# Performance work log

Measured on AMD Instinct MI355X. Metric: run time of the kernel, lower is better.

## Reference

```python
import jax, jax.numpy as jnp
import numpy as np

D_MODEL = 256
D_INNER = 512   # expand_factor * d_model
D_STATE = 64
DT_RANK = 4     # ceil(d_model / 64)
D_CONV = 4
B = 8
L = 144


def setup_inputs() -> dict:
    key = jax.random.key(0)
    ks = jax.random.split(key, 8)
    s = lambda k, shp, sc=0.02: jax.random.normal(k, shp, jnp.float32) * sc
    x = jax.random.normal(ks[0], (B, L, D_MODEL), jnp.float32)
    lastin = jnp.zeros((B, D_INNER, D_STATE), jnp.float32)  # accepted but unused by the scan
    W_in = s(ks[1], (2 * D_INNER, D_MODEL))              # in_proj (no bias)
    conv_w = s(ks[2], (D_INNER, 1, D_CONV), 0.1)          # depthwise conv kernel [O, I/groups, K]
    conv_b = jnp.zeros((D_INNER,), jnp.float32)
    W_x = s(ks[3], (DT_RANK + 2 * D_STATE, D_INNER))      # x_proj (no bias)
    W_dt = s(ks[4], (D_INNER, DT_RANK), 0.1)
    b_dt = jnp.full((D_INNER,), -4.0, jnp.float32)        # softplus -> small dt, like mamba init
    A_log = jnp.log(jnp.tile(jnp.arange(1, D_STATE + 1, dtype=jnp.float32), (D_INNER, 1)))
    Dp = jnp.ones((D_INNER,), jnp.float32)
    W_out = s(ks[5], (D_MODEL, D_INNER))                  # out_proj (no bias)
    return dict(x=x, lastin=lastin, W_in=W_in, conv_w=conv_w, conv_b=conv_b,
                W_x=W_x, W_dt=W_dt, b_dt=b_dt, A_log=A_log, Dp=Dp, W_out=W_out)


def _forward(x, lastin, W_in, conv_w, conv_b, W_x, W_dt, b_dt, A_log, Dp, W_out):
    # in_proj and split
    xz = jnp.einsum('bld,ed->ble', x, W_in)               # [B, L, 2*d_inner]
    ix, z = jnp.split(xz, 2, axis=-1)

    # depthwise causal-ish conv1d: torch padding=2 then slice [:L] == padding (2, 1)
    ix = jnp.swapaxes(ix, 1, 2)                            # [B, d_inner, L]
    ix = jax.lax.conv_general_dilated(
        ix, conv_w, window_strides=(1,), padding=[(2, 1)],
        feature_group_count=D_INNER, dimension_numbers=('NCH', 'OIH', 'NCH'))
    ix = ix + conv_b[None, :, None]
    ix = jnp.swapaxes(ix, 1, 2)                            # [B, L, d_inner]
    ix = jax.nn.silu(ix)

    # ssm parameterization
    A = -jnp.exp(A_log)                                    # [d_inner, d_state]
    dBC = jnp.einsum('bld,ed->ble', ix, W_x)               # [B, L, dt_rank + 2*d_state]
    dt_r = dBC[..., :DT_RANK]
    Bm = dBC[..., DT_RANK:DT_RANK + D_STATE]               # [B, L, d_state]
    Cm = dBC[..., DT_RANK + D_STATE:]                      # [B, L, d_state]
    delta = jax.nn.softplus(jnp.einsum('blr,dr->bld', dt_r, W_dt) + b_dt)  # [B, L, d_inner]

    # discretization
    deltaA = jnp.exp(delta[..., None] * A)                 # [B, L, d_inner, d_state]
    BX = (delta * ix)[..., None] * Bm[:, :, None, :]       # [B, L, d_inner, d_state]

    # sequential selective scan: h_t = deltaA_t * h_{t-1} + BX_t
    def step(h, inp):
        dA_t, bx_t = inp
        h = dA_t * h + bx_t
        return h, h

    h0 = jnp.zeros((x.shape[0], D_INNER, D_STATE), x.dtype)
    _, hs = jax.lax.scan(step, h0, (jnp.moveaxis(deltaA, 1, 0), jnp.moveaxis(BX, 1, 0)))
    # hs: [L, B, d_inner, d_state]

    y = jnp.einsum('lbdn,lbn->bld', hs, jnp.moveaxis(Cm, 1, 0))  # [B, L, d_inner]
    y = y + Dp * ix

    out = jnp.einsum('bld,ed->ble', y * jax.nn.silu(z), W_out)   # [B, L, d_model]
    return out


def reference(x, lastin, W_in, conv_w, conv_b, W_x, W_dt, b_dt, A_log, Dp, W_out):
    return _forward(x, lastin, W_in, conv_w, conv_b, W_x, W_dt, b_dt, A_log, Dp, W_out)
```

## Files before the change

### kernel.cpp

```cpp
#include <hip/hip_runtime.h>
#include <hip/hip_bf16.h>

#define B_SZ 8
#define L_SEQ 144
#define NTOK 1152
#define D_MODEL 256
#define D_INNER 512
#define D_STATE 64
#define DT_RANK 4

#define BM 64
#define BN 64
#define BK 16

template<bool A_MK, bool B_NK, bool GN>
__global__ __launch_bounds__(256) void gemm_k(const float* __restrict__ A,
                                              const float* __restrict__ Bm,
                                              float* __restrict__ C,
                                              const int M, const int N, const int K,
                                              const int lda, const int ldb, const int ldc,
                                              const int kslab, const size_t sstride) {
    __shared__ float As[BK][BM + 4];
    __shared__ float Bs[BK][BN + 4];
    const int tid = threadIdx.x;
    const int m0 = blockIdx.y * BM;
    const int n0 = blockIdx.x * BN;
    const int kbeg = blockIdx.z * kslab;
    const int kend = kbeg + kslab;
    const int ty = tid >> 4, tx = tid & 15;
    const int lrow = tid >> 2, kq = (tid & 3) * 4;
    const int kk = tid >> 4, cc = (tid & 15) * 4;
    float acc[4][4] = {};

    for (int k0 = kbeg; k0 < kend; k0 += BK) {
        float4 av, bv;
        if (A_MK) av = *(const float4*)(A + (size_t)(m0 + lrow) * lda + k0 + kq);
        else      av = *(const float4*)(A + (size_t)(k0 + kk) * lda + m0 + cc);
        if (B_NK) {
            bv = *(const float4*)(Bm + (size_t)(k0 + kk) * ldb + n0 + cc);
        } else {
            bv = make_float4(0.f, 0.f, 0.f, 0.f);
            if (!GN || (n0 + lrow) < N)
                bv = *(const float4*)(Bm + (size_t)(n0 + lrow) * ldb + k0 + kq);
        }
        __syncthreads();
        if (A_MK) {
            As[kq + 0][lrow] = av.x; As[kq + 1][lrow] = av.y;
            As[kq + 2][lrow] = av.z; As[kq + 3][lrow] = av.w;
        } else {
            *(float4*)&As[kk][cc] = av;
        }
        if (B_NK) {
            *(float4*)&Bs[kk][cc] = bv;
        } else {
            Bs[kq + 0][lrow] = bv.x; Bs[kq + 1][lrow] = bv.y;
            Bs[kq + 2][lrow] = bv.z; Bs[kq + 3][lrow] = bv.w;
        }
        __syncthreads();
#pragma unroll
        for (int k = 0; k < BK; ++k) {
            const float4 a4 = *(const float4*)&As[k][ty * 4];
            const float4 b4 = *(const float4*)&Bs[k][tx * 4];
            const float a_[4] = {a4.x, a4.y, a4.z, a4.w};
            const float b_[4] = {b4.x, b4.y, b4.z, b4.w};
#pragma unroll
            for (int i = 0; i < 4; ++i)
#pragma unroll
                for (int j = 0; j < 4; ++j)
                    acc[i][j] = fmaf(a_[i], b_[j], acc[i][j]);
        }
    }
    C += (size_t)blockIdx.z * sstride;
#pragma unroll
    for (int i = 0; i < 4; ++i) {
        const int gm = m0 + ty * 4 + i;
        const int gn = n0 + tx * 4;
        if (!GN || gn < N)
            *(float4*)(C + (size_t)gm * ldc + gn) =
                make_float4(acc[i][0], acc[i][1], acc[i][2], acc[i][3]);
    }
}

__global__ __launch_bounds__(256) void reduce4_k(const float4* __restrict__ in,
                                                 float4* __restrict__ out,
                                                 const int n4, const int s4) {
    const int i = blockIdx.x * 256 + threadIdx.x;
    if (i >= n4) return;
    const float4 a = in[i], b = in[i + s4], c = in[i + 2 * s4], d = in[i + 3 * s4];
    out[i] = make_float4(a.x + b.x + c.x + d.x, a.y + b.y + c.y + d.y,
                         a.z + b.z + c.z + d.z, a.w + b.w + c.w + d.w);
}

__global__ __launch_bounds__(128) void conv_k(const float* __restrict__ xzT,
                                              const float* __restrict__ cw,
                                              const float* __restrict__ cb,
                                              float* __restrict__ ixT) {
    const int tok = blockIdx.x * 128 + threadIdx.x;
    const int d = blockIdx.y;
    const int b = tok / L_SEQ;
    const int t = tok - b * L_SEQ;
    const float* row = xzT + (size_t)d * NTOK + tok;
    const float4 w = *(const float4*)(cw + d * 4);
    float s = cb[d];
    if (t >= 2) s = fmaf(w.x, row[-2], s);
    if (t >= 1) s = fmaf(w.y, row[-1], s);
    s = fmaf(w.z, row[0], s);
    if (t < L_SEQ - 1) s = fmaf(w.w, row[1], s);
    ixT[(size_t)d * NTOK + tok] = s * __builtin_amdgcn_rcpf(1.f + __expf(-s));
}

template<int CNT>
__device__ __forceinline__ void scan_chunk(const float* __restrict__ dBC,
                                           const float* __restrict__ xzT,
                                           const float* __restrict__ ixT,
                                           float* __restrict__ gT,
                                           float4* __restrict__ aux_w,
                                           float (*__restrict__ Pw)[65],
                                           const int d, const int base, const int t0,
                                           const float An2, const float4 wdt,
                                           const float bdt, const float dpv,
                                           const int lane, float& h) {
    if (lane < CNT) {
        const int tok = base + t0 + lane;
        const float4 dt4 = *(const float4*)(dBC + (size_t)tok * 132);
        float s = fmaf(dt4.x, wdt.x, bdt);
        s = fmaf(dt4.y, wdt.y, s);
        s = fmaf(dt4.z, wdt.z, s);
        s = fmaf(dt4.w, wdt.w, s);
        const float delta = fmaxf(s, 0.f) + __logf(1.f + __expf(-fabsf(s)));
        const float ixv = ixT[(size_t)d * NTOK + tok];
        const float zv  = xzT[(size_t)(D_INNER + d) * NTOK + tok];
        const float sz  = zv * __builtin_amdgcn_rcpf(1.f + __expf(-zv));
        aux_w[lane] = make_float4(delta, delta * ixv, dpv * ixv, sz);
    }
#pragma unroll 8
    for (int i = 0; i < CNT; ++i) {
        const size_t rb = (size_t)(base + t0 + i) * 132;
        const float Bv = dBC[rb + DT_RANK + lane];
        const float Cv = dBC[rb + DT_RANK + D_STATE + lane];
        const float4 a4 = aux_w[i];
        const float dA = __builtin_amdgcn_exp2f(a4.x * An2);
        h = fmaf(dA, h, a4.y * Bv);
        Pw[i][lane] = h * Cv;
    }
    const int tl = lane & 31, hf = lane >> 5;
    float s2 = 0.f;
    if (tl < CNT) {
#pragma unroll
        for (int j = 0; j < 32; ++j) s2 += Pw[tl][hf * 32 + j];
    }
    s2 += __shfl_xor(s2, 32, 64);
    if (hf == 0 && tl < CNT) {
        const float4 a4 = aux_w[tl];
        gT[(size_t)d * NTOK + base + t0 + tl] = (s2 + a4.z) * a4.w;
    }
}

__global__ __launch_bounds__(256) void scan_k(const float* __restrict__ dBC,
                                              const float* __restrict__ xzT,
                                              const float* __restrict__ ixT,
                                              const float* __restrict__ W_dt,
                                              const float* __restrict__ b_dt,
                                              const float* __restrict__ A_log,
                                              const float* __restrict__ Dp,
                                              float* __restrict__ gT) {
    __shared__ float4 aux_s[4][32];
    __shared__ float P[4][32][65];
    const int w = threadIdx.x >> 6, lane = threadIdx.x & 63;
    const int b = blockIdx.x >> 7, dg = blockIdx.x & 127;
    const int d = (dg << 2) | w;
    const int base = b * L_SEQ;
    const float An2 = -__expf(A_log[(d << 6) + lane]) * 1.44269504088896f;
    const float4 wdt = *(const float4*)(W_dt + (d << 2));
    const float bdt = b_dt[d], dpv = Dp[d];
    float h = 0.f;
    scan_chunk<32>(dBC, xzT, ixT, gT, aux_s[w], P[w], d, base, 0,  An2, wdt, bdt, dpv, lane, h);
    scan_chunk<32>(dBC, xzT, ixT, gT, aux_s[w], P[w], d, base, 32, An2, wdt, bdt, dpv, lane, h);
    scan_chunk<32>(dBC, xzT, ixT, gT, aux_s[w], P[w], d, base, 64, An2, wdt, bdt, dpv, lane, h);
    scan_chunk<32>(dBC, xzT, ixT, gT, aux_s[w], P[w], d, base, 96, An2, wdt, bdt, dpv, lane, h);
    scan_chunk<16>(dBC, xzT, ixT, gT, aux_s[w], P[w], d, base, 128, An2, wdt, bdt, dpv, lane, h);
}

extern "C" void kernel_launch(void* const* d_in, const int* in_sizes, int n_in,
                              void* d_out, int out_size, void* d_ws, size_t ws_size,
                              hipStream_t stream) {
    const float* x      = (const float*)d_in[0];
    const float* W_in   = (const float*)d_in[2];
    const float* conv_w = (const float*)d_in[3];
    const float* conv_b = (const float*)d_in[4];
    const float* W_x    = (const float*)d_in[5];
    const float* W_dt   = (const float*)d_in[6];
    const float* b_dt   = (const float*)d_in[7];
    const float* A_log  = (const float*)d_in[8];
    const float* Dp     = (const float*)d_in[9];
    const float* W_out  = (const float*)d_in[10];
    float* out = (float*)d_out;

    float* ws    = (float*)d_ws;
    float* xzT   = ws;
    float* ixT   = xzT + 1179648;
    float* dBC   = ixT + 589824;
    float* gT    = dBC + 152064;
    float* slab3 = gT + 589824;
    float* slab6 = xzT;

    gemm_k<true, false, false><<<dim3(18, 16, 1), 256, 0, stream>>>(
        W_in, x, xzT, 1024, NTOK, D_MODEL, D_MODEL, D_MODEL, NTOK, D_MODEL, 0);
    conv_k<<<dim3(9, D_INNER), 128, 0, stream>>>(xzT, conv_w, conv_b, ixT);
    gemm_k<false, false, true><<<dim3(3, 18, 4), 256, 0, stream>>>(
        ixT, W_x, slab3, NTOK, 132, D_INNER, NTOK, D_INNER, 132, 128, (size_t)NTOK * 132);
    reduce4_k<<<dim3(149), 256, 0, stream>>>((const float4*)slab3, (float4*)dBC,
                                             NTOK * 132 / 4, NTOK * 132 / 4);
    scan_k<<<dim3(B_SZ * 128), 256, 0, stream>>>(dBC, xzT, ixT, W_dt, b_dt, A_log, Dp, gT);
    gemm_k<false, false, false><<<dim3(4, 18, 4), 256, 0, stream>>>(
        gT, W_out, slab6, NTOK, D_MODEL, D_INNER, NTOK, D_INNER, D_MODEL, 128,
        (size_t)NTOK * D_MODEL);
    reduce4_k<<<dim3(288), 256, 0, stream>>>((const float4*)slab6, (float4*)out,
                                             NTOK * D_MODEL / 4, NTOK * D_MODEL / 4);
}
```

Baseline: 141.0 us.

## Replace FP32 SIMT GEMMs with split-bf16 MFMA GEMMs and transpose-pack kernels

Swaps the scalar FP32 tiled GEMM for an MFMA kernel that splits each FP32 operand into high and low bf16 parts and accumulates three bf16 products, approximating FP32 accuracy on matrix cores. The activations for the x_proj and out_proj GEMMs are first transposed and packed into hi/lo bf16 pairs by a new transpack kernel. The split-K slabs and reduce kernels are removed. This adds two transpose passes and loses some precision compared with true FP32, and the GEMMs now run without split-K, so they launch fewer blocks.

```diff
diff --git a/kernel.cpp b/kernel.cpp
--- a/kernel.cpp
+++ b/kernel.cpp
@@ -9,86 +9,150 @@
 #define D_STATE 64
 #define DT_RANK 4
 
-#define BM 64
-#define BN 64
-#define BK 16
-
-template<bool A_MK, bool B_NK, bool GN>
-__global__ __launch_bounds__(256) void gemm_k(const float* __restrict__ A,
-                                              const float* __restrict__ Bm,
-                                              float* __restrict__ C,
-                                              const int M, const int N, const int K,
-                                              const int lda, const int ldb, const int ldc,
-                                              const int kslab, const size_t sstride) {
-    __shared__ float As[BK][BM + 4];
-    __shared__ float Bs[BK][BN + 4];
+typedef __attribute__((ext_vector_type(8))) short bf16x8;
+typedef __attribute__((ext_vector_type(4))) float f32x4;
+typedef __attribute__((ext_vector_type(4))) short short4v;
+
+__device__ __forceinline__ unsigned short bf16_rn(float f) {
+    unsigned u = __float_as_uint(f);
+    u += 0x7FFF + ((u >> 16) & 1);
+    return (unsigned short)(u >> 16);
+}
+__device__ __forceinline__ float bf16_f(unsigned short h) {
+    return __uint_as_float(((unsigned)h) << 16);
+}
+__device__ __forceinline__ unsigned packsplit(float f) {
+    const unsigned short h = bf16_rn(f);
+    const unsigned short l = bf16_rn(f - bf16_f(h));
+    return (unsigned)h | ((unsigned)l << 16);
+}
+
+#define LP 40
+
+template<bool APACK, bool GN>
+__global__ __launch_bounds__(256) void gemm_mfma(const void* __restrict__ Aptr,
+                                                 const float* __restrict__ Bptr,
+                                                 float* __restrict__ C,
+                                                 const int N, const int K,
+                                                 const int lda, const int ldb,
+                                                 const int ldc) {
+    __shared__ short Ah[64 * LP], Al[64 * LP], Bh[64 * LP], Bl[64 * LP];
+    const float* Af = (const float*)Aptr;
+    const unsigned* Au = (const unsigned*)Aptr;
     const int tid = threadIdx.x;
-    const int m0 = blockIdx.y * BM;
-    const int n0 = blockIdx.x * BN;
-    const int kbeg = blockIdx.z * kslab;
-    const int kend = kbeg + kslab;
-    const int ty = tid >> 4, tx = tid & 15;
-    const int lrow = tid >> 2, kq = (tid & 3) * 4;
-    const int kk = tid >> 4, cc = (tid & 15) * 4;
-    float acc[4][4] = {};
-
-    for (int k0 = kbeg; k0 < kend; k0 += BK) {
-        float4 av, bv;
-        if (A_MK) av = *(const float4*)(A + (size_t)(m0 + lrow) * lda + k0 + kq);
-        else      av = *(const float4*)(A + (size_t)(k0 + kk) * lda + m0 + cc);
-        if (B_NK) {
-            bv = *(const float4*)(Bm + (size_t)(k0 + kk) * ldb + n0 + cc);
-        } else {
-            bv = make_float4(0.f, 0.f, 0.f, 0.f);
-            if (!GN || (n0 + lrow) < N)
-                bv = *(const float4*)(Bm + (size_t)(n0 + lrow) * ldb + k0 + kq);
+    const int m0 = blockIdx.y * 64;
+    const int n0 = blockIdx.x * 64;
+    const int w = tid >> 6, l = tid & 63;
+    const int lm = l & 15, lq = l >> 4;
+    const int m0w = (w >> 1) * 32, n0w = (w & 1) * 32;
+    f32x4 acc[2][2] = {};
+
+    for (int k0 = 0; k0 < K; k0 += 32) {
+        unsigned short ha[2][4], la[2][4], hb[2][4], lb[2][4];
+#pragma unroll
+        for (int p = 0; p < 2; ++p) {
+            const int i = tid + 256 * p;
+            const int r = i >> 3, c = (i & 7) * 4;
+            if (APACK) {
+                const uint4 v = *(const uint4*)(Au + (size_t)(m0 + r) * lda + k0 + c);
+                ha[p][0] = v.x & 0xFFFF; la[p][0] = v.x >> 16;
+                ha[p][1] = v.y & 0xFFFF; la[p][1] = v.y >> 16;
+                ha[p][2] = v.z & 0xFFFF; la[p][2] = v.z >> 16;
+                ha[p][3] = v.w & 0xFFFF; la[p][3] = v.w >> 16;
+            } else {
+                const float4 v = *(const float4*)(Af + (size_t)(m0 + r) * lda + k0 + c);
+                ha[p][0] = bf16_rn(v.x); la[p][0] = bf16_rn(v.x - bf16_f(ha[p][0]));
+                ha[p][1] = bf16_rn(v.y); la[p][1] = bf16_rn(v.y - bf16_f(ha[p][1]));
+                ha[p][2] = bf16_rn(v.z); la[p][2] = bf16_rn(v.z - bf16_f(ha[p][2]));
+                ha[p][3] = bf16_rn(v.w); la[p][3] = bf16_rn(v.w - bf16_f(ha[p][3]));
+            }
+            float4 bv = make_float4(0.f, 0.f, 0.f, 0.f);
+            if (!GN || (n0 + r) < N)
+                bv = *(const float4*)(Bptr + (size_t)(n0 + r) * ldb + k0 + c);
+            hb[p][0] = bf16_rn(bv.x); lb[p][0] = bf16_rn(bv.x - bf16_f(hb[p][0]));
+            hb[p][1] = bf16_rn(bv.y); lb[p][1] = bf16_rn(bv.y - bf16_f(hb[p][1]));
+            hb[p][2] = bf16_rn(bv.z); lb[p][2] = bf16_rn(bv.z - bf16_f(hb[p][2]));
+            hb[p][3] = bf16_rn(bv.w); lb[p][3] = bf16_rn(bv.w - bf16_f(hb[p][3]));
         }
         __syncthreads();
-        if (A_MK) {
-            As[kq + 0][lrow] = av.x; As[kq + 1][lrow] = av.y;
-            As[kq + 2][lrow] = av.z; As[kq + 3][lrow] = av.w;
-        } else {
-            *(float4*)&As[kk][cc] = av;
-        }
-        if (B_NK) {
-            *(float4*)&Bs[kk][cc] = bv;
-        } else {
-            Bs[kq + 0][lrow] = bv.x; Bs[kq + 1][lrow] = bv.y;
-            Bs[kq + 2][lrow] = bv.z; Bs[kq + 3][lrow] = bv.w;
+#pragma unroll
+        for (int p = 0; p < 2; ++p) {
+            const int i = tid + 256 * p;
+            const int r = i >> 3, c = (i & 7) * 4;
+            const int o = r * LP + c;
+            short4v v;
+            v = (short4v){(short)ha[p][0], (short)ha[p][1], (short)ha[p][2], (short)ha[p][3]};
+            *(short4v*)&Ah[o] = v;
+            v = (short4v){(short)la[p][0], (short)la[p][1], (short)la[p][2], (short)la[p][3]};
+            *(short4v*)&Al[o] = v;
+            v = (short4v){(short)hb[p][0], (short)hb[p][1], (short)hb[p][2], (short)hb[p][3]};
+            *(short4v*)&Bh[o] = v;
+            v = (short4v){(short)lb[p][0], (short)lb[p][1], (short)lb[p][2], (short)lb[p][3]};
+            *(short4v*)&Bl[o] = v;
         }
         __syncthreads();
-#pragma unroll
-        for (int k = 0; k < BK; ++k) {
-            const float4 a4 = *(const float4*)&As[k][ty * 4];
-            const float4 b4 = *(const float4*)&Bs[k][tx * 4];
-            const float a_[4] = {a4.x, a4.y, a4.z, a4.w};
-            const float b_[4] = {b4.x, b4.y, b4.z, b4.w};
-#pragma unroll
-            for (int i = 0; i < 4; ++i)
-#pragma unroll
-                for (int j = 0; j < 4; ++j)
-                    acc[i][j] = fmaf(a_[i], b_[j], acc[i][j]);
-        }
-    }
-    C += (size_t)blockIdx.z * sstride;
-#pragma unroll
-    for (int i = 0; i < 4; ++i) {
-        const int gm = m0 + ty * 4 + i;
-        const int gn = n0 + tx * 4;
-        if (!GN || gn < N)
-            *(float4*)(C + (size_t)gm * ldc + gn) =
-                make_float4(acc[i][0], acc[i][1], acc[i][2], acc[i][3]);
-    }
-}
-
-__global__ __launch_bounds__(256) void reduce4_k(const float4* __restrict__ in,
-                                                 float4* __restrict__ out,
-                                                 const int n4, const int s4) {
-    const int i = blockIdx.x * 256 + threadIdx.x;
-    if (i >= n4) return;
-    const float4 a = in[i], b = in[i + s4], c = in[i + 2 * s4], d = in[i + 3 * s4];
-    out[i] = make_float4(a.x + b.x + c.x + d.x, a.y + b.y + c.y + d.y,
-                         a.z + b.z + c.z + d.z, a.w + b.w + c.w + d.w);
+        bf16x8 fah[2], fal[2], fbh[2], fbl[2];
+#pragma unroll
+        for (int t = 0; t < 2; ++t) {
+            const int ao = (m0w + t * 16 + lm) * LP + lq * 8;
+            fah[t] = *(const bf16x8*)&Ah[ao];
+            fal[t] = *(const bf16x8*)&Al[ao];
+            const int bo = (n0w + t * 16 + lm) * LP + lq * 8;
+            fbh[t] = *(const bf16x8*)&Bh[bo];
+            fbl[t] = *(const bf16x8*)&Bl[bo];
+        }
+#pragma unroll
+        for (int mt = 0; mt < 2; ++mt)
+#pragma unroll
+            for (int nt = 0; nt < 2; ++nt) {
+                acc[mt][nt] = __builtin_amdgcn_mfma_f32_16x16x32_bf16(
+                    fal[mt], fbh[nt], acc[mt][nt], 0, 0, 0);
+                acc[mt][nt] = __builtin_amdgcn_mfma_f32_16x16x32_bf16(
+                    fah[mt], fbl[nt], acc[mt][nt], 0, 0, 0);
+                acc[mt][nt] = __builtin_amdgcn_mfma_f32_16x16x32_bf16(
+                    fah[mt], fbh[nt], acc[mt][nt], 0, 0, 0);
+            }
+    }
+#pragma unroll
+    for (int mt = 0; mt < 2; ++mt) {
+        const int gm = m0 + m0w + mt * 16 + lq * 4;
+#pragma unroll
+        for (int nt = 0; nt < 2; ++nt) {
+            const int gn = n0 + n0w + nt * 16 + lm;
+            if (!GN || gn < N) {
+#pragma unroll
+                for (int r = 0; r < 4; ++r)
+                    C[(size_t)(gm + r) * ldc + gn] = acc[mt][nt][r];
+            }
+        }
+    }
+}
+
+__global__ __launch_bounds__(256) void transpack_k(const float* __restrict__ in,
+                                                   unsigned* __restrict__ out) {
+    __shared__ unsigned T[64][65];
+    const int t0 = blockIdx.x * 64, d0 = blockIdx.y * 64;
+    const int a = threadIdx.x & 15, g = threadIdx.x >> 4;
+#pragma unroll
+    for (int p = 0; p < 4; ++p) {
+        const int d = g + 16 * p;
+        const float4 v = *(const float4*)(in + (size_t)(d0 + d) * NTOK + t0 + a * 4);
+        T[d][a * 4 + 0] = packsplit(v.x);
+        T[d][a * 4 + 1] = packsplit(v.y);
+        T[d][a * 4 + 2] = packsplit(v.z);
+        T[d][a * 4 + 3] = packsplit(v.w);
+    }
+    __syncthreads();
+#pragma unroll
+    for (int p = 0; p < 4; ++p) {
+        const int tt = g + 16 * p;
+        uint4 o;
+        o.x = T[a * 4 + 0][tt];
+        o.y = T[a * 4 + 1][tt];
+        o.z = T[a * 4 + 2][tt];
+        o.w = T[a * 4 + 3][tt];
+        *(uint4*)(out + (size_t)(t0 + tt) * D_INNER + d0 + a * 4) = o;
+    }
 }
 
 __global__ __launch_bounds__(128) void conv_k(const float* __restrict__ xzT,
@@ -196,25 +260,22 @@
     const float* W_out  = (const float*)d_in[10];
     float* out = (float*)d_out;
 
-    float* ws    = (float*)d_ws;
-    float* xzT   = ws;
-    float* ixT   = xzT + 1179648;
-    float* dBC   = ixT + 589824;
-    float* gT    = dBC + 152064;
-    float* slab3 = gT + 589824;
-    float* slab6 = xzT;
-
-    gemm_k<true, false, false><<<dim3(18, 16, 1), 256, 0, stream>>>(
-        W_in, x, xzT, 1024, NTOK, D_MODEL, D_MODEL, D_MODEL, NTOK, D_MODEL, 0);
+    float* ws  = (float*)d_ws;
+    float* xzT = ws;
+    float* ixT = xzT + 1179648;
+    float* dBC = ixT + 589824;
+    float* gT  = dBC + 152064;
+    unsigned* ixM = (unsigned*)(gT + 589824);
+    unsigned* gM  = ixM + 589824;
+
+    gemm_mfma<false, false><<<dim3(18, 16), 256, 0, stream>>>(
+        W_in, x, xzT, NTOK, D_MODEL, D_MODEL, D_MODEL, NTOK);
     conv_k<<<dim3(9, D_INNER), 128, 0, stream>>>(xzT, conv_w, conv_b, ixT);
-    gemm_k<false, false, true><<<dim3(3, 18, 4), 256, 0, stream>>>(
-        ixT, W_x, slab3, NTOK, 132, D_INNER, NTOK, D_INNER, 132, 128, (size_t)NTOK * 132);
-    reduce4_k<<<dim3(149), 256, 0, stream>>>((const float4*)slab3, (float4*)dBC,
-                                             NTOK * 132 / 4, NTOK * 132 / 4);
+    transpack_k<<<dim3(18, 8), 256, 0, stream>>>(ixT, ixM);
+    gemm_mfma<true, true><<<dim3(3, 18), 256, 0, stream>>>(
+        ixM, W_x, dBC, 132, D_INNER, D_INNER, D_INNER, 132);
     scan_k<<<dim3(B_SZ * 128), 256, 0, stream>>>(dBC, xzT, ixT, W_dt, b_dt, A_log, Dp, gT);
-    gemm_k<false, false, false><<<dim3(4, 18, 4), 256, 0, stream>>>(
-        gT, W_out, slab6, NTOK, D_MODEL, D_INNER, NTOK, D_INNER, D_MODEL, 128,
-        (size_t)NTOK * D_MODEL);
-    reduce4_k<<<dim3(288), 256, 0, stream>>>((const float4*)slab6, (float4*)out,
-                                             NTOK * D_MODEL / 4, NTOK * D_MODEL / 4);
-}
+    transpack_k<<<dim3(18, 8), 256, 0, stream>>>(gT, gM);
+    gemm_mfma<true, false><<<dim3(4, 18), 256, 0, stream>>>(
+        gM, W_out, out, D_MODEL, D_INNER, D_INNER, D_INNER, D_MODEL);
+}
```

Result: slower. 144.1 us (+2.2%).
